# Optimization experiments

Hardware: AMD Instinct MI355X
Metric: run time of the kernel (lower is better)

## Reference

```python
import jax, jax.numpy as jnp
import numpy as np

B = 16          # graphs per batch
T = 50          # cell types
C = 200         # neurons per cell type
N = T * C       # nodes per graph (10000)
NT = B * N      # total nodes (160000)
FEAT = 1        # num_node_features (forced to 1 by module structure)
H = 8           # attention heads
DEG = 32
E = NT * DEG    # edges (5.12M)
PASSES = 4
PERSIST = 1.0
EPS = 1e-5
TAU = 1.0
SLOPE = 0.2


def setup_inputs() -> dict:
    key = jax.random.key(0)
    ks = jax.random.split(key, 12)
    x = jax.random.normal(ks[0], (NT, FEAT), dtype=jnp.float32)
    # sprinkle exact zeros so the noise-injection branch is exercised
    x = jnp.where(jax.random.uniform(ks[1], x.shape) < 0.1, 0.0, x)
    # edges stay within each graph (batched disjoint graphs)
    dst = jax.random.randint(ks[2], (E,), 0, NT)
    src = (dst // N) * N + jax.random.randint(ks[3], (E,), 0, N)
    edge_index = jnp.stack([src, dst]).astype(jnp.int32)
    batch = (jnp.arange(NT) // N).astype(jnp.int32)
    perm_weights = jax.random.normal(ks[4], (T, B, C, C), dtype=jnp.float32)
    decision_vec = (jax.random.uniform(ks[5], (N,)) < 0.2).astype(jnp.float32)
    gat_w = jax.random.normal(ks[6], (FEAT, H), dtype=jnp.float32)
    att_src = jax.random.normal(ks[7], (H,), dtype=jnp.float32)
    att_dst = jax.random.normal(ks[8], (H,), dtype=jnp.float32)
    return {
        "x": x, "edge_index": edge_index, "batch": batch,
        "perm_weights": perm_weights, "decision_vec": decision_vec,
        "gat_w": gat_w, "att_src": att_src, "att_dst": att_dst,
        "gat_bias": jnp.zeros((1,), jnp.float32),
        "bn_gamma": jnp.ones((1,), jnp.float32),
        "bn_beta": jnp.zeros((1,), jnp.float32),
        "bn_mean": jnp.zeros((1,), jnp.float32),
        "bn_var": jnp.ones((1,), jnp.float32),
        "lin_w": jax.random.normal(ks[9], (1, 1), dtype=jnp.float32),
        "lin_b": jax.random.normal(ks[10], (1,), dtype=jnp.float32),
    }


def _permutation_layer(x, perm_weights, key):
    # x: [NT, FEAT] -> per-type blocks [T, B, C, FEAT]
    xb = x.reshape(B, T, C, FEAT).transpose(1, 0, 2, 3)
    u = jax.random.uniform(key, perm_weights.shape, minval=1e-10, maxval=1.0)
    gumbel = -jnp.log(-jnp.log(u))
    # F.gumbel_softmax(weights, dim=1) on [B,C,C] -> softmax over row axis (axis=2 here)
    soft = jax.nn.softmax((perm_weights + gumbel) / TAU, axis=2)
    y = jnp.einsum('tbij,tbjf->tbif', soft, xb)
    return y.transpose(1, 0, 2, 3).reshape(NT, FEAT)


def _add_noise(x, key):
    nz = x != 0
    n = nz.sum().astype(x.dtype)
    mean = jnp.sum(jnp.where(nz, x, 0.0)) / n
    var = jnp.sum(jnp.where(nz, (x - mean) ** 2, 0.0)) / (n - 1.0)  # unbiased, as torch .std()
    std = jnp.sqrt(var)
    noise = (std / 100.0) * jax.random.normal(key, x.shape, dtype=x.dtype)
    return jnp.where(nz, x, noise)


def _gat_conv(x, src, dst, gat_w, att_src, att_dst, gat_bias):
    xs = x @ gat_w                                   # [NT, H] (out_channels=1 per head)
    a_src = xs * att_src                             # [NT, H]
    a_dst = xs * att_dst
    e = a_src[src] + a_dst[dst]                      # [E+NT, H]
    e = jnp.where(e > 0, e, SLOPE * e)               # leaky_relu(0.2)
    emax = jax.ops.segment_max(e, dst, num_segments=NT)
    ee = jnp.exp(e - emax[dst])
    denom = jax.ops.segment_sum(ee, dst, num_segments=NT)
    alpha = ee / denom[dst]
    out = jax.ops.segment_sum(alpha * xs[src], dst, num_segments=NT)  # [NT, H]
    return out.mean(axis=1, keepdims=True) + gat_bias  # concat=False -> mean over heads


def reference(x, edge_index, batch, perm_weights, decision_vec, gat_w, att_src,
              att_dst, gat_bias, bn_gamma, bn_beta, bn_mean, bn_var, lin_w, lin_b):
    rk = jax.random.key(42)
    x = _permutation_layer(x, perm_weights, jax.random.fold_in(rk, 0))
    x_res = x
    x = _add_noise(x, jax.random.fold_in(rk, 1))
    # GATConv adds self loops by default
    loops = jnp.arange(NT, dtype=edge_index.dtype)
    src = jnp.concatenate([edge_index[0], loops])
    dst = jnp.concatenate([edge_index[1], loops])
    for i in range(PASSES):
        x = _gat_conv(x, src, dst, gat_w, att_src, att_dst, gat_bias)
        x = (x - bn_mean) / jnp.sqrt(bn_var + EPS) * bn_gamma + bn_beta  # eval BN
        x = jax.nn.silu(x)
        # dropout is identity in eval mode
        x = x + x_res * (PERSIST ** i)
    mask = jnp.tile(decision_vec, B)[:, None]        # [NT, 1]
    x = x * mask
    pooled = jax.ops.segment_max(x, batch, num_segments=B)  # global_max_pool -> [B, 1]
    return jax.nn.relu(pooled @ lin_w.T + lin_b)
```

## Files before the change

kernel.cpp:

```cpp
#include <hip/hip_runtime.h>
#include <stdint.h>
#include <math.h>

#define B_   16
#define T_   50
#define C_   200
#define N_   10000
#define NT_  160000
#define H_   8
#define E_   5120000
#define EPS_ 1e-5f
#define NB_  625
#define EB_  512
#define EPB_ 10000
#define ATH_ 1024
#define GB_  16
#define GC_  625
#define GTH_ 640
#define JC_  5
#define JW_  40
#define ROWP_ 41
#define BCAP_ 10240
#define LOG2E_ 1.44269504088896340736f

__device__ __forceinline__ float ex2(float x){
  float r; asm("v_exp_f32 %0, %1" : "=v"(r) : "v"(x)); return r;
}
__device__ __forceinline__ float ex2na(float x){
  float r; asm("v_exp_f32 %0, -abs(%1)" : "=v"(r) : "v"(x)); return r;
}
__device__ __forceinline__ float lg2(float x){
  float r; asm("v_log_f32 %0, %1" : "=v"(r) : "v"(x)); return r;
}

__device__ __forceinline__ int wscan_incl(int v, int lane){
#pragma unroll
  for (int d = 1; d < 64; d <<= 1){
    int t = __shfl_up(v, d, 64);
    if (lane >= d) v += t;
  }
  return v;
}

struct TF2C { unsigned a, b; };
constexpr unsigned rotl32c(unsigned v, int r){ return (v << r) | (v >> (32 - r)); }
constexpr TF2C tf_const(unsigned k0, unsigned k1, unsigned x0, unsigned x1){
  unsigned ks2 = k0 ^ k1 ^ 0x1BD11BDAu;
  unsigned ks[3] = {k0, k1, ks2};
  x0 += k0; x1 += k1;
  const int RA[4] = {13, 15, 26, 6};
  const int RB[4] = {17, 29, 16, 24};
  for (int g = 0; g < 5; ++g){
    for (int r = 0; r < 4; ++r){
      int rr = (g & 1) ? RB[r] : RA[r];
      x0 += x1; x1 = rotl32c(x1, rr); x1 ^= x0;
    }
    x0 += ks[(g + 1) % 3];
    x1 += ks[(g + 2) % 3] + (unsigned)(g + 1);
  }
  return TF2C{x0, x1};
}
constexpr TF2C KG = tf_const(0u, 42u, 0u, 0u);
constexpr TF2C KN = tf_const(0u, 42u, 0u, 1u);

#define ROTL_(x, r) __builtin_amdgcn_alignbit((x), (x), 32 - (r))

__device__ __forceinline__ void tf2(unsigned k0, unsigned k1, unsigned x0, unsigned x1,
                                    unsigned &o0, unsigned &o1){
  unsigned ks2 = k0 ^ k1 ^ 0x1BD11BDAu;
  x0 += k0; x1 += k1;
#define TFR_(R) { x0 += x1; x1 = ROTL_(x1, R); x1 ^= x0; }
  TFR_(13) TFR_(15) TFR_(26) TFR_(6)  x0 += k1;  x1 += ks2 + 1u;
  TFR_(17) TFR_(29) TFR_(16) TFR_(24) x0 += ks2; x1 += k0 + 2u;
  TFR_(13) TFR_(15) TFR_(26) TFR_(6)  x0 += k0;  x1 += k1 + 3u;
  TFR_(17) TFR_(29) TFR_(16) TFR_(24) x0 += k1;  x1 += ks2 + 4u;
  TFR_(13) TFR_(15) TFR_(26) TFR_(6)  x0 += ks2; x1 += k0 + 5u;
#undef TFR_
  o0 = x0; o1 = x1;
}
__device__ __forceinline__ unsigned rbits(unsigned ka, unsigned kb, unsigned m){
  unsigned a, b; tf2(ka, kb, 0u, m, a, b); return a ^ b;
}

__device__ __forceinline__ float erfinv_xla(float x){
  float w = -log1pf(-x * x);
  float p;
  if (w < 5.0f){
    w = w - 2.5f;
    p = 2.81022636e-08f;
    p = fmaf(p, w, 3.43273939e-07f);
    p = fmaf(p, w, -3.5233877e-06f);
    p = fmaf(p, w, -4.39150654e-06f);
    p = fmaf(p, w, 0.00021858087f);
    p = fmaf(p, w, -0.00125372503f);
    p = fmaf(p, w, -0.00417768164f);
    p = fmaf(p, w, 0.246640727f);
    p = fmaf(p, w, 1.50140941f);
  } else {
    w = sqrtf(w) - 3.0f;
    p = -0.000200214257f;
    p = fmaf(p, w, 0.000100950558f);
    p = fmaf(p, w, 0.00134934322f);
    p = fmaf(p, w, -0.00367342844f);
    p = fmaf(p, w, 0.00573950773f);
    p = fmaf(p, w, -0.0076224613f);
    p = fmaf(p, w, 0.00943887047f);
    p = fmaf(p, w, 1.00167406f);
    p = fmaf(p, w, 2.83297682f);
  }
  return p * x;
}

__global__ __launch_bounds__(ATH_)
void k_hist(const int* __restrict__ dst, int* __restrict__ cnt){
  __shared__ int h[NB_];
  int tid = threadIdx.x, blk = blockIdx.x;
  for (int i = tid; i < NB_; i += ATH_) h[i] = 0;
  __syncthreads();
  int e0 = blk * EPB_;
  for (int i = tid; i < EPB_; i += ATH_)
    atomicAdd(&h[dst[e0 + i] >> 8], 1);
  __syncthreads();
  for (int i = tid; i < NB_; i += ATH_) cnt[blk * NB_ + i] = h[i];
}

__global__ __launch_bounds__(512)
void k_sumb(const int* __restrict__ cnt, int* __restrict__ bsum){
  __shared__ int sred[8];
  int b = blockIdx.x, tid = threadIdx.x;
  int v = cnt[tid * NB_ + b];
#pragma unroll
  for (int s = 32; s >= 1; s >>= 1) v += __shfl_xor(v, s, 64);
  int w = tid >> 6, l = tid & 63;
  if (l == 0) sred[w] = v;
  __syncthreads();
  if (tid == 0){
    int t = 0;
#pragma unroll
    for (int i = 0; i < 8; ++i) t += sred[i];
    bsum[b] = t;
  }
}

__global__ __launch_bounds__(640)
void k_scanb(const int* __restrict__ bsum, int* __restrict__ boff){
  __shared__ int wsum[16];
  int tid = threadIdx.x, lane = tid & 63, wid = tid >> 6;
  int v = (tid < NB_) ? bsum[tid] : 0;
  int inc = wscan_incl(v, lane);
  if (lane == 63) wsum[wid] = inc;
  __syncthreads();
  if (wid == 0){
    int wv = (lane < 10) ? wsum[lane] : 0;
    int wi = wscan_incl(wv, lane);
    if (lane < 10) wsum[lane] = wi - wv;
  }
  __syncthreads();
  if (tid < NB_) boff[tid] = inc - v + wsum[wid];
  if (tid == 0) boff[NB_] = E_;
}

__global__ __launch_bounds__(512)
void k_scanc(const int* __restrict__ cnt, const int* __restrict__ boff,
             int* __restrict__ gscan){
  __shared__ int wsum[8];
  int b = blockIdx.x, tid = threadIdx.x, lane = tid & 63, wid = tid >> 6;
  int v = cnt[tid * NB_ + b];
  int inc = wscan_incl(v, lane);
  if (lane == 63) wsum[wid] = inc;
  __syncthreads();
  int wp = 0;
#pragma unroll
  for (int k = 0; k < 8; ++k) wp += (k < wid) ? wsum[k] : 0;
  gscan[tid * NB_ + b] = boff[b] + inc - v + wp;
}

__global__ __launch_bounds__(ATH_)
void k_append(const int* __restrict__ src, const int* __restrict__ dst,
              const int* __restrict__ cnt, const int* __restrict__ gscan,
              unsigned* __restrict__ ebuf){
  __shared__ unsigned esh[EPB_];
  __shared__ int loff[NB_ + 1];
  __shared__ int cur[NB_];
  __shared__ int wsum[16];
  int tid = threadIdx.x, blk = blockIdx.x;
  int lane = tid & 63, wid = tid >> 6;
  int e0 = blk * EPB_;
  for (int i = tid; i < NB_; i += ATH_) cur[i] = 0;
  int hv = (tid < NB_) ? cnt[blk * NB_ + tid] : 0;
  int inc = wscan_incl(hv, lane);
  if (lane == 63 && wid < 10) wsum[wid] = inc;
  __syncthreads();
  if (wid == 0){
    int wv = (lane < 10) ? wsum[lane] : 0;
    int wi = wscan_incl(wv, lane);
    if (lane < 10) wsum[lane] = wi - wv;
  }
  __syncthreads();
  if (tid < NB_) loff[tid] = inc - hv + wsum[wid];
  if (tid == 0) loff[NB_] = EPB_;
  __syncthreads();
  for (int i = tid; i < EPB_; i += ATH_){
    int e = e0 + i;
    int d = dst[e];
    int b = d >> 8;
    int p = loff[b] + atomicAdd(&cur[b], 1);
    esh[p] = ((unsigned)src[e] << 8) | (unsigned)(d & 255);
  }
  __syncthreads();
  for (int b = wid; b < NB_; b += ATH_ / 64){
    int lo = loff[b], len = loff[b + 1] - lo;
    int gb0 = gscan[blk * NB_ + b];
    for (int p = lane; p < len; p += 64)
      ebuf[gb0 + p] = esh[lo + p];
  }
}

__global__ __launch_bounds__(512)
void k_bcsr(const int* __restrict__ boff, const unsigned* __restrict__ ebuf,
            int* __restrict__ offs, unsigned short* __restrict__ srcs16){
  __shared__ unsigned esh[BCAP_];
  __shared__ int cnt[256];
  __shared__ int cur[256];
  __shared__ int wsum[4];
  int b = blockIdx.x, tid = threadIdx.x, lane = tid & 63, wid = tid >> 6;
  int e0 = boff[b], e1 = boff[b + 1];
  int len = e1 - e0;
  int base_node = b * 256;
  int offA = (base_node / N_) * N_;
  int boundary = offA + N_;
  bool staged = (len <= BCAP_);
  if (tid < 256) cnt[tid] = 0;
  __syncthreads();
  if (staged){
    for (int e = tid; e < len; e += 512){
      unsigned pk = ebuf[e0 + e];
      esh[e] = pk;
      atomicAdd(&cnt[pk & 255u], 1);
    }
  } else {
    for (int e = tid; e < len; e += 512)
      atomicAdd(&cnt[ebuf[e0 + e] & 255u], 1);
  }
  __syncthreads();
  int v = (tid < 256) ? cnt[tid] : 0;
  int inc = wscan_incl(v, lane);
  if (lane == 63 && wid < 4) wsum[wid] = inc;
  __syncthreads();
  int wp = 0;
#pragma unroll
  for (int k = 0; k < 4; ++k) wp += (k < wid) ? wsum[k] : 0;
  int excl = inc - v + wp;
  if (tid < 256){ offs[base_node + tid] = e0 + excl; cur[tid] = excl; }
  __syncthreads();
  if (staged){
    for (int e = tid; e < len; e += 512){
      unsigned pk = esh[e];
      int dl = (int)(pk & 255u);
      int goff = (base_node + dl >= boundary) ? boundary : offA;
      int pos = e0 + atomicAdd(&cur[dl], 1);
      srcs16[pos] = (unsigned short)((int)(pk >> 8) - goff);
    }
  } else {
    for (int e = tid; e < len; e += 512){
      unsigned pk = ebuf[e0 + e];
      int dl = (int)(pk & 255u);
      int goff = (base_node + dl >= boundary) ? boundary : offA;
      int pos = e0 + atomicAdd(&cur[dl], 1);
      srcs16[pos] = (unsigned short)((int)(pk >> 8) - goff);
    }
  }
  if (b == 0 && tid == 0) offs[NT_] = E_;
}

__global__ __launch_bounds__(512, 8)
void k_perm(const float* __restrict__ W, const float* __restrict__ x,
            float* __restrict__ ypart){
  __shared__ float ez[C_ * ROWP_];
  __shared__ float Ssh[JW_];
  __shared__ float rs[JW_];

  const int bid = blockIdx.x;
  const int tb = bid / JC_;
  const int jc = bid - tb * JC_;
  const int t = tb / B_;
  const int b = tb - t * B_;
  const int j0 = jc * JW_;
  const int xoff = (b * T_ + t) * C_;
  const int tid = threadIdx.x;
  const int w = tid >> 6, l = tid & 63;

  {
    int i  = tid / 10;
    int jq = tid - i * 10;
    unsigned m = (unsigned)(tb * (C_ * C_) + i * C_ + j0 + 4 * jq);
    int la = i * ROWP_ + 4 * jq;
    int niter = (2000 - tid + 511) >> 9;
    for (int it = 0; it < niter; ++it){
      float4 w4 = *reinterpret_cast<const float4*>(W + m);
      unsigned bb0 = rbits(KG.a, KG.b, m);
      unsigned bb1 = rbits(KG.a, KG.b, m + 1u);
      unsigned bb2 = rbits(KG.a, KG.b, m + 2u);
      unsigned bb3 = rbits(KG.a, KG.b, m + 3u);
      unsigned bbv[4] = {bb0, bb1, bb2, bb3};
      float wvv[4] = {w4.x, w4.y, w4.z, w4.w};
#pragma unroll
      for (int k = 0; k < 4; ++k){
        unsigned bits = bbv[k];
        float fc = (float)(bits >> 9);
        float u  = fmaf(fc, 0x1p-23f, 1e-10f);
        float tl = lg2(u) * -0.69314718056f;
        float d  = fmaf(-fc, 0x1p-23f, 1.0f);
        float p  = 0.25f;
        p = fmaf(p, d, 0.33333333f);
        p = fmaf(p, d, 0.5f);
        p = fmaf(p, d, 1.0f);
        float tneg = (bits >= 0xFC000000u) ? d * p : tl;
        ez[la + k] = ex2(wvv[k] * LOG2E_) * __builtin_amdgcn_rcpf(tneg);
      }
      jq += 2;
      int wrap = jq >= 10;
      jq = wrap ? jq - 10 : jq;
      m  += wrap ? 10368u : 10208u;
      la += wrap ? 2100 : 2099;
    }
  }
  __syncthreads();

#pragma unroll
  for (int q = 0; q < 5; ++q){
    int jj = w * 5 + q;
    float s = ez[l * ROWP_ + jj] + ez[(l + 64) * ROWP_ + jj] + ez[(l + 128) * ROWP_ + jj]
            + ((l < 8) ? ez[(l + 192) * ROWP_ + jj] : 0.f);
#pragma unroll
    for (int sh = 32; sh >= 1; sh >>= 1) s += __shfl_xor(s, sh, 64);
    if (l == 0) Ssh[jj] = s;
  }
  __syncthreads();
  if (tid < JW_) rs[tid] = x[xoff + j0 + tid] / Ssh[tid];
  __syncthreads();

  if (tid < C_){
    float acc = 0.f;
#pragma unroll 8
    for (int jj = 0; jj < JW_; ++jj)
      acc = fmaf(ez[tid * ROWP_ + jj], rs[jj], acc);
    ypart[jc * NT_ + xoff + tid] = acc;
  }
}

__global__ __launch_bounds__(256)
void k_ycomb(const float* __restrict__ ypart, float* __restrict__ y,
             float* __restrict__ spart){
  __shared__ float sred[12];
  int n = blockIdx.x * 256 + threadIdx.x;
  float v = 0.f;
#pragma unroll
  for (int jc = 0; jc < JC_; ++jc) v += ypart[jc * NT_ + n];
  y[n] = v;
  float s = 0.f, c = 0.f, q = 0.f;
  if (v != 0.f){ s = v; c = 1.f; q = v * v; }
#pragma unroll
  for (int sh = 32; sh >= 1; sh >>= 1){
    s += __shfl_xor(s, sh, 64);
    c += __shfl_xor(c, sh, 64);
    q += __shfl_xor(q, sh, 64);
  }
  int w = threadIdx.x >> 6, l = threadIdx.x & 63;
  if (l == 0){ sred[w] = s; sred[4 + w] = c; sred[8 + w] = q; }
  __syncthreads();
  if (threadIdx.x == 0){
    spart[blockIdx.x * 3 + 0] = sred[0] + sred[1] + sred[2] + sred[3];
    spart[blockIdx.x * 3 + 1] = sred[4] + sred[5] + sred[6] + sred[7];
    spart[blockIdx.x * 3 + 2] = sred[8] + sred[9] + sred[10] + sred[11];
  }
}

template<int MODE>
__global__ __launch_bounds__(GTH_)
void k_gat(const float* __restrict__ xin, const float* __restrict__ xres,
           const int* __restrict__ offs, const unsigned short* __restrict__ srcs16,
           const float* __restrict__ gw, const float* __restrict__ asrc,
           const float* __restrict__ adst, const float* __restrict__ gbias,
           const float* __restrict__ bng, const float* __restrict__ bnb,
           const float* __restrict__ bnm, const float* __restrict__ bnv,
           const float* __restrict__ spart, const float* __restrict__ dv,
           float* __restrict__ xout, float* __restrict__ pmax){
  __shared__ float xsh[N_];
  __shared__ float sred3[32];
  int g = blockIdx.x / GB_, c = blockIdx.x - g * GB_;
  int tid = threadIdx.x;
  if (MODE == 1){
    float s = 0.f, cc = 0.f, q = 0.f;
    for (int i = tid; i < 625; i += GTH_){
      s += spart[i * 3 + 0]; cc += spart[i * 3 + 1]; q += spart[i * 3 + 2];
    }
#pragma unroll
    for (int sh = 32; sh >= 1; sh >>= 1){
      s += __shfl_xor(s, sh, 64);
      cc += __shfl_xor(cc, sh, 64);
      q += __shfl_xor(q, sh, 64);
    }
    int wv2 = tid >> 6, l2 = tid & 63;
    if (l2 == 0){ sred3[wv2] = s; sred3[10 + wv2] = cc; sred3[20 + wv2] = q; }
    __syncthreads();
    float S = 0.f, C2 = 0.f, Q = 0.f;
#pragma unroll
    for (int k = 0; k < 10; ++k){ S += sred3[k]; C2 += sred3[10 + k]; Q += sred3[20 + k]; }
    float scale = sqrtf((Q - S * S / C2) / (C2 - 1.f)) * 0.01f;
    for (int i = tid; i < N_; i += GTH_){
      float v = xin[g * N_ + i];
      if (v == 0.0f){
        unsigned bits = rbits(KN.a, KN.b, (unsigned)(g * N_ + i));
        float f = __uint_as_float((bits >> 9) | 0x3f800000u) - 1.0f;
        float u = fmaf(f, 2.0f, -0.99999994f);
        u = fmaxf(-0.99999994f, u);
        v = scale * 1.41421356237f * erfinv_xla(u);
      }
      xsh[i] = v;
    }
  } else {
    const float4* xv = (const float4*)(xin + g * N_);
    for (int i = tid; i < N_ / 4; i += GTH_) ((float4*)xsh)[i] = xv[i];
  }
  __syncthreads();

  bool act = tid < GC_;
  int nl = c * GC_ + (act ? tid : 0);
  int n = g * N_ + nl;
  float xn = xsh[nl];

  float cs[H_], cdxn[H_], wv[H_];
#pragma unroll
  for (int h = 0; h < H_; ++h){
    wv[h] = gw[h];
    cs[h] = wv[h] * asrc[h] * LOG2E_;
    cdxn[h] = wv[h] * adst[h] * xn * LOG2E_;
  }
  float mh[H_], den[H_], num[H_];
#pragma unroll
  for (int h = 0; h < H_; ++h){
    float v = cs[h] * xn + cdxn[h];
    v = fmaxf(v, 0.2f * v);
    mh[h] = v; den[h] = 1.f; num[h] = xn;
  }
  int e0 = offs[n], e1 = act ? offs[n + 1] : e0;

  int e = e0;
  if ((e < e1) && (e & 1)){
    float xs = xsh[srcs16[e]];
#pragma unroll
    for (int h = 0; h < H_; ++h){
      float v = fmaf(cs[h], xs, cdxn[h]);
      v = fmaxf(v, 0.2f * v);
      float d = v - mh[h];
      float ed = ex2na(d);
      bool nm = d > 0.f;
      float corr = nm ? ed : 1.f;
      float p    = nm ? 1.f : ed;
      mh[h] = fmaxf(mh[h], v);
      den[h] = fmaf(den[h], corr, p);
      num[h] = fmaf(num[h], corr, p * xs);
    }
    ++e;
  }
  for (; e + 1 < e1; e += 2){
    unsigned pr = *reinterpret_cast<const unsigned*>(srcs16 + e);
    float xa = xsh[pr & 0xFFFFu];
    float xb = xsh[pr >> 16];
#pragma unroll
    for (int h = 0; h < H_; ++h){
      float va = fmaf(cs[h], xa, cdxn[h]);  va = fmaxf(va, 0.2f * va);
      float vb = fmaf(cs[h], xb, cdxn[h]);  vb = fmaxf(vb, 0.2f * vb);
      float m2 = fmaxf(va, vb);
      float ed2 = ex2na(va - vb);
      bool bmx = vb > va;
      float xmx = bmx ? xb : xa;
      float xmn = bmx ? xa : xb;
      float den2 = 1.0f + ed2;
      float num2 = fmaf(ed2, xmn, xmx);
      float d = m2 - mh[h];
      float ed = ex2na(d);
      bool nm = d > 0.f;
      float corr = nm ? ed : 1.f;
      float p    = nm ? 1.f : ed;
      mh[h] = fmaxf(mh[h], m2);
      den[h] = fmaf(den[h], corr, p * den2);
      num[h] = fmaf(num[h], corr, p * num2);
    }
  }
  if (e < e1){
    float xs = xsh[srcs16[e]];
#pragma unroll
    for (int h = 0; h < H_; ++h){
      float v = fmaf(cs[h], xs, cdxn[h]);
      v = fmaxf(v, 0.2f * v);
      float d = v - mh[h];
      float ed = ex2na(d);
      bool nm = d > 0.f;
      float corr = nm ? ed : 1.f;
      float p    = nm ? 1.f : ed;
      mh[h] = fmaxf(mh[h], v);
      den[h] = fmaf(den[h], corr, p);
      num[h] = fmaf(num[h], corr, p * xs);
    }
  }

  float o = 0.f;
#pragma unroll
  for (int h = 0; h < H_; ++h) o += wv[h] * num[h] * __builtin_amdgcn_rcpf(den[h]);
  o = o * 0.125f + gbias[0];
  o = (o - bnm[0]) / sqrtf(bnv[0] + EPS_) * bng[0] + bnb[0];
  o = o / (1.0f + __expf(-o));
  float res = o + xres[n];

  if (MODE == 2){
    float m2 = act ? res * dv[nl] : -INFINITY;
#pragma unroll
    for (int s = 32; s >= 1; s >>= 1) m2 = fmaxf(m2, __shfl_xor(m2, s, 64));
    int wv2 = tid >> 6, l2 = tid & 63;
    if (l2 == 0) sred3[wv2] = m2;
    __syncthreads();
    if (tid == 0){
      float p = sred3[0];
#pragma unroll
      for (int i2 = 1; i2 < 10; ++i2) p = fmaxf(p, sred3[i2]);
      pmax[blockIdx.x] = p;
    }
  } else {
    if (act) xout[n] = res;
  }
}

__global__ void k_pool2(const float* __restrict__ pmax, const float* __restrict__ lw,
                        const float* __restrict__ lb, float* __restrict__ out){
  int b = blockIdx.x, l = threadIdx.x;
  float m = (l < GB_) ? pmax[b * GB_ + l] : -INFINITY;
#pragma unroll
  for (int s = 32; s >= 1; s >>= 1) m = fmaxf(m, __shfl_xor(m, s, 64));
  if (l == 0){
    float o = m * lw[0] + lb[0];
    out[b] = (o > 0.f) ? o : 0.f;
  }
}

extern "C" void kernel_launch(void* const* d_in, const int* in_sizes, int n_in,
                              void* d_out, int out_size, void* d_ws, size_t ws_size,
                              hipStream_t stream){
  const float* x     = (const float*)d_in[0];
  const int*   ei    = (const int*)d_in[1];
  const float* W     = (const float*)d_in[3];
  const float* dv    = (const float*)d_in[4];
  const float* gw    = (const float*)d_in[5];
  const float* asrc  = (const float*)d_in[6];
  const float* adst  = (const float*)d_in[7];
  const float* gbias = (const float*)d_in[8];
  const float* bng   = (const float*)d_in[9];
  const float* bnb   = (const float*)d_in[10];
  const float* bnm   = (const float*)d_in[11];
  const float* bnv   = (const float*)d_in[12];
  const float* lw    = (const float*)d_in[13];
  const float* lb    = (const float*)d_in[14];
  float* out = (float*)d_out;

  char* ws = (char*)d_ws;
  int*            offs   = (int*)           (ws + 0);
  unsigned short* srcs16 = (unsigned short*)(ws + 640256);
  int*            cnt    = (int*)           (ws + 10880256);
  int*            gscan  = (int*)           (ws + 12160256);
  unsigned*       ebuf   = (unsigned*)      (ws + 21120256);
  float*          ypart  = (float*)         (ws + 21120256);
  float*          y      = (float*)         (ws + 41600256);
  float*          x0     = (float*)         (ws + 42240256);
  float*          x1     = (float*)         (ws + 42880256);
  int*            bsum   = (int*)           (ws + 43520256);
  int*            boff   = (int*)           (ws + 43522816);
  float*          pmax   = (float*)         (ws + 43525376);
  float*          spart  = (float*)         (ws + 43527968);
  if (ws_size < (size_t)43535500) return;

  const int* esrc = ei;
  const int* edst = ei + E_;

  k_hist  <<<EB_, ATH_, 0, stream>>>(edst, cnt);
  k_sumb  <<<NB_, 512, 0, stream>>>(cnt, bsum);
  k_scanb <<<1, 640, 0, stream>>>(bsum, boff);
  k_scanc <<<NB_, 512, 0, stream>>>(cnt, boff, gscan);
  k_append<<<EB_, ATH_, 0, stream>>>(esrc, edst, cnt, gscan, ebuf);
  k_bcsr  <<<NB_, 512, 0, stream>>>(boff, ebuf, offs, srcs16);
  k_perm  <<<T_ * B_ * JC_, 512, 0, stream>>>(W, x, ypart);
  k_ycomb <<<625, 256, 0, stream>>>(ypart, y, spart);
  k_gat<1><<<B_ * GB_, GTH_, 0, stream>>>(y,  y, offs, srcs16, gw, asrc, adst, gbias, bng, bnb, bnm, bnv, spart, dv, x1, pmax);
  k_gat<0><<<B_ * GB_, GTH_, 0, stream>>>(x1, y, offs, srcs16, gw, asrc, adst, gbias, bng, bnb, bnm, bnv, spart, dv, x0, pmax);
  k_gat<0><<<B_ * GB_, GTH_, 0, stream>>>(x0, y, offs, srcs16, gw, asrc, adst, gbias, bng, bnb, bnm, bnv, spart, dv, x1, pmax);
  k_gat<2><<<B_ * GB_, GTH_, 0, stream>>>(x1, y, offs, srcs16, gw, asrc, adst, gbias, bng, bnb, bnm, bnv, spart, dv, x0, pmax);
  k_pool2 <<<B_, 64, 0, stream>>>(pmax, lw, lb, out);
}
```

Baseline: 293.4 us.

## Fuse bucket-sum into histogram via atomics and prefetch next edge pair in GAT loop

The separate k_sumb reduction kernel is removed. Each k_hist block now atomically adds its per-bucket counts into bsum, which a memset zeroes beforehand. This saves a kernel launch and a strided re-read of cnt, at the cost of global atomics. Separately, the GAT pair loop is software-pipelined: it loads the next pair's source indices and x values before computing the current pair, which hides shared-memory and index load latency but uses more registers.

```diff
diff --git a/kernel.cpp b/kernel.cpp
--- a/kernel.cpp
+++ b/kernel.cpp
@@ -112,7 +112,8 @@
 }
 
 __global__ __launch_bounds__(ATH_)
-void k_hist(const int* __restrict__ dst, int* __restrict__ cnt){
+void k_hist(const int* __restrict__ dst, int* __restrict__ cnt,
+            int* __restrict__ bsum){
   __shared__ int h[NB_];
   int tid = threadIdx.x, blk = blockIdx.x;
   for (int i = tid; i < NB_; i += ATH_) h[i] = 0;
@@ -121,24 +122,10 @@
   for (int i = tid; i < EPB_; i += ATH_)
     atomicAdd(&h[dst[e0 + i] >> 8], 1);
   __syncthreads();
-  for (int i = tid; i < NB_; i += ATH_) cnt[blk * NB_ + i] = h[i];
-}
-
-__global__ __launch_bounds__(512)
-void k_sumb(const int* __restrict__ cnt, int* __restrict__ bsum){
-  __shared__ int sred[8];
-  int b = blockIdx.x, tid = threadIdx.x;
-  int v = cnt[tid * NB_ + b];
-#pragma unroll
-  for (int s = 32; s >= 1; s >>= 1) v += __shfl_xor(v, s, 64);
-  int w = tid >> 6, l = tid & 63;
-  if (l == 0) sred[w] = v;
-  __syncthreads();
-  if (tid == 0){
-    int t = 0;
-#pragma unroll
-    for (int i = 0; i < 8; ++i) t += sred[i];
-    bsum[b] = t;
+  for (int i = tid; i < NB_; i += ATH_){
+    int v = h[i];
+    cnt[blk * NB_ + i] = v;
+    if (v) atomicAdd(&bsum[i], v);
   }
 }
 
@@ -464,30 +451,40 @@
     }
     ++e;
   }
-  for (; e + 1 < e1; e += 2){
+  int npairs = (e1 - e) >> 1;
+  if (npairs > 0){
     unsigned pr = *reinterpret_cast<const unsigned*>(srcs16 + e);
     float xa = xsh[pr & 0xFFFFu];
     float xb = xsh[pr >> 16];
-#pragma unroll
-    for (int h = 0; h < H_; ++h){
-      float va = fmaf(cs[h], xa, cdxn[h]);  va = fmaxf(va, 0.2f * va);
-      float vb = fmaf(cs[h], xb, cdxn[h]);  vb = fmaxf(vb, 0.2f * vb);
-      float m2 = fmaxf(va, vb);
-      float ed2 = ex2na(va - vb);
-      bool bmx = vb > va;
-      float xmx = bmx ? xb : xa;
-      float xmn = bmx ? xa : xb;
-      float den2 = 1.0f + ed2;
-      float num2 = fmaf(ed2, xmn, xmx);
-      float d = m2 - mh[h];
-      float ed = ex2na(d);
-      bool nm = d > 0.f;
-      float corr = nm ? ed : 1.f;
-      float p    = nm ? 1.f : ed;
-      mh[h] = fmaxf(mh[h], m2);
-      den[h] = fmaf(den[h], corr, p * den2);
-      num[h] = fmaf(num[h], corr, p * num2);
-    }
+    for (int it = 0; it < npairs; ++it){
+      int en = e + 2 * it + 2;
+      en = (it + 1 < npairs) ? en : e;
+      unsigned prn = *reinterpret_cast<const unsigned*>(srcs16 + en);
+      float xan = xsh[prn & 0xFFFFu];
+      float xbn = xsh[prn >> 16];
+#pragma unroll
+      for (int h = 0; h < H_; ++h){
+        float va = fmaf(cs[h], xa, cdxn[h]);  va = fmaxf(va, 0.2f * va);
+        float vb = fmaf(cs[h], xb, cdxn[h]);  vb = fmaxf(vb, 0.2f * vb);
+        float m2 = fmaxf(va, vb);
+        float ed2 = ex2na(va - vb);
+        bool bmx = vb > va;
+        float xmx = bmx ? xb : xa;
+        float xmn = bmx ? xa : xb;
+        float den2 = 1.0f + ed2;
+        float num2 = fmaf(ed2, xmn, xmx);
+        float d = m2 - mh[h];
+        float ed = ex2na(d);
+        bool nm = d > 0.f;
+        float corr = nm ? ed : 1.f;
+        float p    = nm ? 1.f : ed;
+        mh[h] = fmaxf(mh[h], m2);
+        den[h] = fmaf(den[h], corr, p * den2);
+        num[h] = fmaf(num[h], corr, p * num2);
+      }
+      xa = xan; xb = xbn;
+    }
+    e += 2 * npairs;
   }
   if (e < e1){
     float xs = xsh[srcs16[e]];
@@ -582,8 +579,8 @@
   const int* esrc = ei;
   const int* edst = ei + E_;
 
-  k_hist  <<<EB_, ATH_, 0, stream>>>(edst, cnt);
-  k_sumb  <<<NB_, 512, 0, stream>>>(cnt, bsum);
+  hipMemsetAsync(bsum, 0, NB_ * sizeof(int), stream);
+  k_hist  <<<EB_, ATH_, 0, stream>>>(edst, cnt, bsum);
   k_scanb <<<1, 640, 0, stream>>>(bsum, boff);
   k_scanc <<<NB_, 512, 0, stream>>>(cnt, boff, gscan);
   k_append<<<EB_, ATH_, 0, stream>>>(esrc, edst, cnt, gscan, ebuf);
```

After: 305.5 us. +4.1%, slower.
